# Kernel optimization log

Measured on AMD Instinct MI355X. Metric: run time of the kernel, lower is better.

The kernel has to match this reference:

```python
import jax, jax.numpy as jnp
import numpy as np

# Static module configuration (mirrors torch __init__ args)
P, T = 5, 16                # p_bins, t_bins
B = P * T                   # 80 rotational/radial bins
C_IN, R_IN = 16, 1
C_OUT, R_OUT = 32, 16
N_VERTS = 20000             # mesh vertices (conn is sparse (N_VERTS*B, N_VERTS))
NNZ = 6400000               # nonzeros in conn
K = C_IN * R_IN * B         # flattened kernel-support size = 1280


def _rotation_matrix():
    """Static int index table, identical to EquivariantLayer.rotate."""
    def angle_rot(v):
        # pif_1[i*t : i*t+t-1] = pif[i*t+1 : i*t+t]; wrap last -> roll -1 over t axis
        return np.roll(v.reshape(R_IN, T, P), -1, axis=1).reshape(-1)

    def kernel_rot(v):
        # pif_1[1:] = pif[:-1]; pif_1[0] = pif[-1] -> roll +1 over R_IN axis
        return np.roll(v.reshape(R_IN, T * P), 1, axis=0).reshape(-1)

    small = np.zeros((R_IN * T * P, R_OUT), dtype=np.int64)
    pif = np.arange(R_IN * T * P, dtype=np.int64)
    small[:, 0] = pif
    for j in range(1, R_OUT):
        pif = kernel_rot(angle_rot(pif))
        small[:, j] = pif
    # tile over input channels with per-channel offsets
    offs = (np.arange(C_IN, dtype=np.int64) * R_IN * T * P)[:, None, None]
    return (small[None, :, :] + offs).reshape(K, R_OUT)

ROT = jnp.asarray(_rotation_matrix())  # (K, R_OUT) constant indices


def setup_inputs() -> dict:
    key = jax.random.key(0)
    k1, k2, k3, k4, k5 = jax.random.split(key, 5)
    x = jax.random.normal(k1, (N_VERTS, C_IN * R_IN), dtype=jnp.float32)
    weights = jax.random.normal(k2, (C_OUT, K), dtype=jnp.float32)
    conn_vals = jax.random.uniform(k3, (NNZ,), dtype=jnp.float32)
    conn_rows = jax.random.randint(k4, (NNZ,), 0, N_VERTS * B)  # dest (vertex,bin) row
    conn_cols = jax.random.randint(k5, (NNZ,), 0, N_VERTS)      # source vertex
    return {"x": x, "weights": weights, "conn_vals": conn_vals,
            "conn_rows": conn_rows, "conn_cols": conn_cols}


def reference(x, weights, conn_vals, conn_rows, conn_cols):
    # 1) build layer_weights via gather over all C_out rows at once:
    #    layer_weights[:, i*R_out:(i+1)*R_out] = weights[i][ROT]
    lw = weights[:, ROT]                          # (C_out, K, R_out)
    lw = jnp.transpose(lw, (1, 0, 2)).reshape(K, C_OUT * R_OUT)  # (K, C_out*R_out)
    # 2) sparse.mm(conn, x): gather source features, scale, scatter-add to (vertex,bin) rows
    msg = conn_vals[:, None] * x[conn_cols]       # (NNZ, C_in*R_in)
    agg = jax.ops.segment_sum(msg, conn_rows, num_segments=N_VERTS * B)  # (N*B, C_in*R_in)
    # 3) reshape to per-vertex flattened kernel support and dense matmul
    h = agg.reshape(-1, B * C_IN * R_IN)          # (N, K)
    return h @ lw                                 # (N, C_out*R_out)
```

## Files before the change

kernel.cpp:

```cpp
#include <hip/hip_runtime.h>

#define NV 20000
#define NNZE 6400000
#define KD 1280
#define ND 512
#define MROWS 20000
#define MPAD 20096

typedef __attribute__((ext_vector_type(8))) short short8;
typedef __attribute__((ext_vector_type(4))) float f32x4;

static const size_t AGG_ELEMS = (size_t)MPAD * KD;

static __device__ __forceinline__ unsigned short f2bf(float f) {
    unsigned int u = __float_as_uint(f);
    unsigned int r = (u + 0x7FFFu + ((u >> 16) & 1u)) >> 16;
    return (unsigned short)r;
}

__global__ void zero_kernel(float4* __restrict__ p, long long n4) {
    long long i = (long long)blockIdx.x * blockDim.x + threadIdx.x;
    long long stride = (long long)gridDim.x * blockDim.x;
    for (; i < n4; i += stride) p[i] = make_float4(0.f, 0.f, 0.f, 0.f);
}

__global__ void build_lwT_kernel(const float* __restrict__ w, unsigned short* __restrict__ lwT) {
    int idx = blockIdx.x * blockDim.x + threadIdx.x;
    int n = idx / KD;
    int k = idx - n * KD;
    int o = n >> 4, j = n & 15;
    int ci = k / 80;
    int i  = k - ci * 80;
    int t  = i / 5, p = i - t * 5;
    int src = ci * 80 + ((t + j) & 15) * 5 + p;
    lwT[idx] = f2bf(w[o * KD + src]);
}

__global__ __launch_bounds__(256) void scatter_kernel(
        const float* __restrict__ vals, const int* __restrict__ rows,
        const int* __restrict__ cols, const float* __restrict__ x,
        float* __restrict__ agg) {
    long long idx = (long long)blockIdx.x * 256 + threadIdx.x;
    if (idx >= (long long)NNZE * 16) return;
    int e = (int)(idx >> 4);
    int c = (int)(idx & 15);
    int r  = rows[e];
    int cl = cols[e];
    float v = vals[e];
    atomicAdd(agg + ((long long)r << 4) + c, v * x[(cl << 4) + c]);
}

__global__ __launch_bounds__(256) void gemm_kernel(
        const float* __restrict__ A, const unsigned short* __restrict__ lwT,
        float* __restrict__ C) {
    __shared__ __align__(16) char lds[2 * 128 * 64 * 2];
    char* As = lds;
    char* Bs = lds + 128 * 64 * 2;

    int tid  = threadIdx.x;
    int lane = tid & 63;
    int wid  = tid >> 6;
    int wr = wid >> 1, wc = wid & 1;
    int m0 = blockIdx.x * 128;
    int n0 = blockIdx.y * 128;

    int l15 = lane & 15;
    int l4  = lane >> 4;

    f32x4 acc[4][4] = {};

    int arow  = tid >> 1;
    int ahalf = tid & 1;
    const float* aptr = A + (size_t)(m0 + arow) * KD + ahalf * 32;
    int aswz = (arow & 7) << 4;

    for (int k0 = 0; k0 < KD; k0 += 64) {
        float4 av[8];
#pragma unroll
        for (int q = 0; q < 8; q++)
            av[q] = ((const float4*)(aptr + k0))[q];

#pragma unroll
        for (int rd = 0; rd < 4; rd++) {
            int idx  = rd * 256 + tid;
            int brow = idx >> 3;
            int cb   = (idx & 7) * 16;
            size_t src = (size_t)(n0 + brow) * (KD * 2) + (size_t)(k0 * 2)
                       + (size_t)(cb ^ ((brow & 7) << 4));
            __builtin_amdgcn_global_load_lds(
                (const __attribute__((address_space(1))) void*)((const char*)lwT + src),
                (__attribute__((address_space(3))) void*)(Bs + rd * 4096 + wid * 1024),
                16, 0, 0);
        }

#pragma unroll
        for (int q = 0; q < 4; q++) {
            short8 s;
            s[0] = (short)f2bf(av[2*q].x);   s[1] = (short)f2bf(av[2*q].y);
            s[2] = (short)f2bf(av[2*q].z);   s[3] = (short)f2bf(av[2*q].w);
            s[4] = (short)f2bf(av[2*q+1].x); s[5] = (short)f2bf(av[2*q+1].y);
            s[6] = (short)f2bf(av[2*q+1].z); s[7] = (short)f2bf(av[2*q+1].w);
            int cb = ahalf * 64 + q * 16;
            *(short8*)(As + arow * 128 + (cb ^ aswz)) = s;
        }

        __syncthreads();

#pragma unroll
        for (int ks = 0; ks < 2; ks++) {
            short8 af[4], bf[4];
            int kb = ks * 64 + l4 * 16;
#pragma unroll
            for (int m = 0; m < 4; m++) {
                int r = wr * 64 + m * 16 + l15;
                af[m] = *(const short8*)(As + r * 128 + (kb ^ ((r & 7) << 4)));
            }
#pragma unroll
            for (int n = 0; n < 4; n++) {
                int r = wc * 64 + n * 16 + l15;
                bf[n] = *(const short8*)(Bs + r * 128 + (kb ^ ((r & 7) << 4)));
            }
#pragma unroll
            for (int m = 0; m < 4; m++)
#pragma unroll
                for (int n = 0; n < 4; n++)
                    acc[m][n] = __builtin_amdgcn_mfma_f32_16x16x32_bf16(
                                    af[m], bf[n], acc[m][n], 0, 0, 0);
        }

        __syncthreads();
    }

#pragma unroll
    for (int m = 0; m < 4; m++) {
        int row_b = m0 + wr * 64 + m * 16 + l4 * 4;
#pragma unroll
        for (int n = 0; n < 4; n++) {
            int col = n0 + wc * 64 + n * 16 + l15;
#pragma unroll
            for (int r = 0; r < 4; r++) {
                int row = row_b + r;
                if (row < MROWS) C[(size_t)row * ND + col] = acc[m][n][r];
            }
        }
    }
}

extern "C" void kernel_launch(void* const* d_in, const int* in_sizes, int n_in,
                              void* d_out, int out_size, void* d_ws, size_t ws_size,
                              hipStream_t stream) {
    const float* x         = (const float*)d_in[0];
    const float* weights   = (const float*)d_in[1];
    const float* conn_vals = (const float*)d_in[2];
    const int*   conn_rows = (const int*)d_in[3];
    const int*   conn_cols = (const int*)d_in[4];
    float* out = (float*)d_out;

    float*          agg = (float*)d_ws;
    unsigned short* lwT = (unsigned short*)((char*)d_ws + AGG_ELEMS * 4);

    hipLaunchKernelGGL(zero_kernel, dim3(4096), dim3(256), 0, stream,
                       (float4*)agg, (long long)(AGG_ELEMS / 4));
    hipLaunchKernelGGL(build_lwT_kernel, dim3((ND * KD) / 256), dim3(256), 0, stream,
                       weights, lwT);
    long long total = (long long)NNZE * 16;
    hipLaunchKernelGGL(scatter_kernel, dim3((unsigned)((total + 255) / 256)), dim3(256),
                       0, stream, conn_vals, conn_rows, conn_cols, x, agg);
    hipLaunchKernelGGL(gemm_kernel, dim3(MPAD / 128, ND / 128), dim3(256), 0, stream,
                       agg, lwT, out);
}
```

Measured before the change: 627.5 us.

## Replace atomic scatter with counting-sort CSR build and per-row gather

Drops the per-element float atomic scatter into a large fp32 aggregation buffer. Instead, each of two halves of the destination rows gets a histogram, a two-level prefix scan and a reorder of (value, column) pairs into row-sorted order. A gather kernel then sums each row's messages in registers and writes bf16 directly. The GEMM now streams bf16 A tiles with global_load_lds instead of converting fp32 in registers. This trades contended atomics and a large zeroing pass for several extra passes over the index arrays and scattered writes during the reorder.

```diff
diff --git a/kernel.cpp b/kernel.cpp
--- a/kernel.cpp
+++ b/kernel.cpp
@@ -5,27 +5,26 @@
 #define KD 1280
 #define ND 512
 #define MROWS 20000
-#define MPAD 20096
+#define NR 1600000
+#define HALF 800000
+#define NBLK 391
 
 typedef __attribute__((ext_vector_type(8))) short short8;
 typedef __attribute__((ext_vector_type(4))) float f32x4;
 
-static const size_t AGG_ELEMS = (size_t)MPAD * KD;
-
 static __device__ __forceinline__ unsigned short f2bf(float f) {
     unsigned int u = __float_as_uint(f);
-    unsigned int r = (u + 0x7FFFu + ((u >> 16) & 1u)) >> 16;
-    return (unsigned short)r;
-}
-
-__global__ void zero_kernel(float4* __restrict__ p, long long n4) {
-    long long i = (long long)blockIdx.x * blockDim.x + threadIdx.x;
-    long long stride = (long long)gridDim.x * blockDim.x;
-    for (; i < n4; i += stride) p[i] = make_float4(0.f, 0.f, 0.f, 0.f);
-}
-
-__global__ void build_lwT_kernel(const float* __restrict__ w, unsigned short* __restrict__ lwT) {
-    int idx = blockIdx.x * blockDim.x + threadIdx.x;
+    return (unsigned short)((u + 0x7FFFu + ((u >> 16) & 1u)) >> 16);
+}
+
+__global__ __launch_bounds__(256) void zero_u32(unsigned int* __restrict__ p, int n) {
+    int i = blockIdx.x * 256 + threadIdx.x;
+    if (i < n) p[i] = 0u;
+}
+
+__global__ __launch_bounds__(256) void build_lwT_kernel(
+        const float* __restrict__ w, unsigned short* __restrict__ lwT) {
+    int idx = blockIdx.x * 256 + threadIdx.x;
     int n = idx / KD;
     int k = idx - n * KD;
     int o = n >> 4, j = n & 15;
@@ -36,26 +35,94 @@
     lwT[idx] = f2bf(w[o * KD + src]);
 }
 
-__global__ __launch_bounds__(256) void scatter_kernel(
-        const float* __restrict__ vals, const int* __restrict__ rows,
-        const int* __restrict__ cols, const float* __restrict__ x,
-        float* __restrict__ agg) {
-    long long idx = (long long)blockIdx.x * 256 + threadIdx.x;
-    if (idx >= (long long)NNZE * 16) return;
-    int e = (int)(idx >> 4);
-    int c = (int)(idx & 15);
-    int r  = rows[e];
-    int cl = cols[e];
-    float v = vals[e];
-    atomicAdd(agg + ((long long)r << 4) + c, v * x[(cl << 4) + c]);
+__global__ __launch_bounds__(256) void hist_kernel(
+        const int* __restrict__ rows, unsigned int* __restrict__ A, int lo, int hi) {
+    int e = blockIdx.x * 256 + threadIdx.x;
+    int r = rows[e];
+    if (r >= lo && r < hi) atomicAdd(&A[r - lo], 1u);
+}
+
+__global__ __launch_bounds__(256) void scan1_kernel(
+        unsigned int* __restrict__ A, unsigned int* __restrict__ bsum) {
+    __shared__ unsigned int sh[256];
+    int tid  = threadIdx.x;
+    int base = blockIdx.x * 2048 + tid * 8;
+    unsigned int v[8];
+    unsigned int run = 0;
+#pragma unroll
+    for (int q = 0; q < 8; q++) {
+        unsigned int t = (base + q < HALF) ? A[base + q] : 0u;
+        v[q] = run;
+        run += t;
+    }
+    sh[tid] = run;
+    __syncthreads();
+    unsigned int own = run;
+    for (int ofs = 1; ofs < 256; ofs <<= 1) {
+        unsigned int t = (tid >= ofs) ? sh[tid - ofs] : 0u;
+        __syncthreads();
+        sh[tid] += t;
+        __syncthreads();
+    }
+    unsigned int excl = sh[tid] - own;
+#pragma unroll
+    for (int q = 0; q < 8; q++)
+        if (base + q < HALF) A[base + q] = excl + v[q];
+    if (tid == 255) bsum[blockIdx.x] = sh[255];
+}
+
+__global__ __launch_bounds__(512) void scan2_kernel(unsigned int* __restrict__ bsum) {
+    __shared__ unsigned int sh[512];
+    int tid = threadIdx.x;
+    unsigned int v = (tid < NBLK) ? bsum[tid] : 0u;
+    sh[tid] = v;
+    __syncthreads();
+    for (int ofs = 1; ofs < 512; ofs <<= 1) {
+        unsigned int t = (tid >= ofs) ? sh[tid - ofs] : 0u;
+        __syncthreads();
+        sh[tid] += t;
+        __syncthreads();
+    }
+    if (tid < NBLK) bsum[tid] = sh[tid] - v;
+}
+
+__global__ __launch_bounds__(256) void reorder_kernel(
+        const int* __restrict__ rows, const float* __restrict__ vals,
+        const int* __restrict__ cols, unsigned int* __restrict__ A,
+        const unsigned int* __restrict__ bsum, uint2* __restrict__ sorted,
+        int lo, int hi) {
+    int e = blockIdx.x * 256 + threadIdx.x;
+    int r = rows[e];
+    if (r >= lo && r < hi) {
+        int i = r - lo;
+        unsigned int pos = bsum[i >> 11] + atomicAdd(&A[i], 1u);
+        sorted[pos] = make_uint2(__float_as_uint(vals[e]), (unsigned int)cols[e]);
+    }
+}
+
+__global__ __launch_bounds__(256) void gather_kernel(
+        const uint2* __restrict__ sorted, const unsigned int* __restrict__ A,
+        const unsigned int* __restrict__ bsum, const float* __restrict__ x,
+        unsigned short* __restrict__ agg, int lo) {
+    int gt = blockIdx.x * 256 + threadIdx.x;
+    int i  = gt >> 4;
+    int ch = gt & 15;
+    unsigned int start = (i > 0) ? (A[i - 1] + bsum[(i - 1) >> 11]) : 0u;
+    unsigned int end   = A[i] + bsum[i >> 11];
+    float acc = 0.f;
+    for (unsigned int p = start; p < end; p++) {
+        uint2 s = sorted[p];
+        acc = fmaf(__uint_as_float(s.x), x[(s.y << 4) + ch], acc);
+    }
+    agg[((size_t)(lo + i) << 4) + ch] = f2bf(acc);
 }
 
 __global__ __launch_bounds__(256) void gemm_kernel(
-        const float* __restrict__ A, const unsigned short* __restrict__ lwT,
+        const unsigned short* __restrict__ Abf, const unsigned short* __restrict__ lwT,
         float* __restrict__ C) {
     __shared__ __align__(16) char lds[2 * 128 * 64 * 2];
     char* As = lds;
-    char* Bs = lds + 128 * 64 * 2;
+    char* Bs = lds + 16384;
 
     int tid  = threadIdx.x;
     int lane = tid & 63;
@@ -63,45 +130,30 @@
     int wr = wid >> 1, wc = wid & 1;
     int m0 = blockIdx.x * 128;
     int n0 = blockIdx.y * 128;
-
     int l15 = lane & 15;
     int l4  = lane >> 4;
 
     f32x4 acc[4][4] = {};
 
-    int arow  = tid >> 1;
-    int ahalf = tid & 1;
-    const float* aptr = A + (size_t)(m0 + arow) * KD + ahalf * 32;
-    int aswz = (arow & 7) << 4;
-
     for (int k0 = 0; k0 < KD; k0 += 64) {
-        float4 av[8];
-#pragma unroll
-        for (int q = 0; q < 8; q++)
-            av[q] = ((const float4*)(aptr + k0))[q];
-
 #pragma unroll
         for (int rd = 0; rd < 4; rd++) {
             int idx  = rd * 256 + tid;
-            int brow = idx >> 3;
+            int trow = idx >> 3;
             int cb   = (idx & 7) * 16;
-            size_t src = (size_t)(n0 + brow) * (KD * 2) + (size_t)(k0 * 2)
-                       + (size_t)(cb ^ ((brow & 7) << 4));
+            int swz  = cb ^ ((trow & 7) << 4);
+            int gr   = m0 + trow;
+            if (gr > MROWS - 1) gr = MROWS - 1;
+            size_t asrc = (size_t)gr * (KD * 2) + (size_t)(k0 * 2) + swz;
             __builtin_amdgcn_global_load_lds(
-                (const __attribute__((address_space(1))) void*)((const char*)lwT + src),
+                (const __attribute__((address_space(1))) void*)((const char*)Abf + asrc),
+                (__attribute__((address_space(3))) void*)(As + rd * 4096 + wid * 1024),
+                16, 0, 0);
+            size_t bsrc = (size_t)(n0 + trow) * (KD * 2) + (size_t)(k0 * 2) + swz;
+            __builtin_amdgcn_global_load_lds(
+                (const __attribute__((address_space(1))) void*)((const char*)lwT + bsrc),
                 (__attribute__((address_space(3))) void*)(Bs + rd * 4096 + wid * 1024),
                 16, 0, 0);
-        }
-
-#pragma unroll
-        for (int q = 0; q < 4; q++) {
-            short8 s;
-            s[0] = (short)f2bf(av[2*q].x);   s[1] = (short)f2bf(av[2*q].y);
-            s[2] = (short)f2bf(av[2*q].z);   s[3] = (short)f2bf(av[2*q].w);
-            s[4] = (short)f2bf(av[2*q+1].x); s[5] = (short)f2bf(av[2*q+1].y);
-            s[6] = (short)f2bf(av[2*q+1].z); s[7] = (short)f2bf(av[2*q+1].w);
-            int cb = ahalf * 64 + q * 16;
-            *(short8*)(As + arow * 128 + (cb ^ aswz)) = s;
         }
 
         __syncthreads();
@@ -156,16 +208,29 @@
     const int*   conn_cols = (const int*)d_in[4];
     float* out = (float*)d_out;
 
-    float*          agg = (float*)d_ws;
-    unsigned short* lwT = (unsigned short*)((char*)d_ws + AGG_ELEMS * 4);
-
-    hipLaunchKernelGGL(zero_kernel, dim3(4096), dim3(256), 0, stream,
-                       (float4*)agg, (long long)(AGG_ELEMS / 4));
+    char* ws = (char*)d_ws;
+    unsigned short* agg    = (unsigned short*)ws;
+    uint2*          sorted = (uint2*)(ws + 51200000);
+    unsigned int*   A      = (unsigned int*)(ws + 77600000);
+    unsigned int*   bsum   = (unsigned int*)(ws + 80800000);
+    unsigned short* lwT    = (unsigned short*)(ws + 80802048);
+
     hipLaunchKernelGGL(build_lwT_kernel, dim3((ND * KD) / 256), dim3(256), 0, stream,
                        weights, lwT);
-    long long total = (long long)NNZE * 16;
-    hipLaunchKernelGGL(scatter_kernel, dim3((unsigned)((total + 255) / 256)), dim3(256),
-                       0, stream, conn_vals, conn_rows, conn_cols, x, agg);
-    hipLaunchKernelGGL(gemm_kernel, dim3(MPAD / 128, ND / 128), dim3(256), 0, stream,
-                       agg, lwT, out);
-}
+
+    for (int pass = 0; pass < 2; pass++) {
+        int lo = pass * HALF, hi = lo + HALF;
+        hipLaunchKernelGGL(zero_u32, dim3(HALF / 256 + 1), dim3(256), 0, stream, A, HALF);
+        hipLaunchKernelGGL(hist_kernel, dim3(NNZE / 256), dim3(256), 0, stream,
+                           conn_rows, A, lo, hi);
+        hipLaunchKernelGGL(scan1_kernel, dim3(NBLK), dim3(256), 0, stream, A, bsum);
+        hipLaunchKernelGGL(scan2_kernel, dim3(1), dim3(512), 0, stream, bsum);
+        hipLaunchKernelGGL(reorder_kernel, dim3(NNZE / 256), dim3(256), 0, stream,
+                           conn_rows, conn_vals, conn_cols, A, bsum, sorted, lo, hi);
+        hipLaunchKernelGGL(gather_kernel, dim3((HALF * 16) / 256), dim3(256), 0, stream,
+                           sorted, A, bsum, x, agg, lo);
+    }
+
+    hipLaunchKernelGGL(gemm_kernel, dim3((MROWS + 127) / 128, ND / 128), dim3(256),
+                       0, stream, agg, lwT, out);
+}
```

After: 999.4 us. +59.3%, slower.
